# Kernel tuning notes

Hardware: AMD Instinct MI355X
Metric: run time of the kernel (lower is better)

The kernel has to match this reference:

```python
import jax, jax.numpy as jnp
import numpy as np

N_KNOTS = 16
DEGREE = 3
N_BASES = N_KNOTS - DEGREE - 1  # 12
F_CH = 128
KNOTS = jnp.linspace(0.0, 2.0, N_KNOTS, dtype=jnp.float32)


def bspline_basis(x, knots, degree):
    """Cox-de Boor B-spline basis. x: [...], returns [..., K-degree-1]."""
    K = knots.shape[0]
    xe = x[..., None]
    # degree-0 indicator basis: [..., K-1]
    b = ((xe >= knots[:-1]) & (xe < knots[1:])).astype(x.dtype)
    for d in range(1, degree + 1):
        left_den = knots[d:K - 1] - knots[:K - d - 1]
        right_den = knots[d + 1:K] - knots[1:K - d]
        safe_l = jnp.where(left_den > 0, left_den, 1.0)
        safe_r = jnp.where(right_den > 0, right_den, 1.0)
        left = jnp.where(left_den > 0, (xe - knots[:K - d - 1]) / safe_l, 0.0)
        right = jnp.where(right_den > 0, (knots[d + 1:K] - xe) / safe_r, 0.0)
        b = left * b[..., :K - d - 1] + right * b[..., 1:K - d]
    return b  # [..., K-degree-1]


def setup_inputs() -> dict:
    key = jax.random.key(0)
    k1, k2, k3 = jax.random.split(key, 3)
    B, N = 32, 8192
    eval_x = jax.random.normal(k1, (B, N, F_CH), dtype=jnp.float32)
    eval_eigs = jax.random.uniform(k2, (B, N), dtype=jnp.float32)  # in [0,1) within knot span [0,2]
    filter_scale = 1.0
    filter_coeffs = jax.random.normal(k3, (N_BASES, F_CH), dtype=jnp.float32) * filter_scale
    return {"eval_x": eval_x, "eval_eigs": eval_eigs, "filter_coeffs": filter_coeffs}


def reference(eval_x, eval_eigs, filter_coeffs):
    # basis: [B, N, n_bases]
    basis = bspline_basis(eval_eigs, KNOTS, DEGREE)
    # The torch split/cat/bmm/stack/transpose chain is exactly this contraction:
    # spectral_filter[b,n,f] = sum_k basis[b,n,k] * coeffs[k,f]
    spectral_filter = jnp.einsum('bnk,kf->bnf', basis, filter_coeffs)
    return eval_x * jnp.square(spectral_filter)
```

## Files before the change

kernel.cpp:

```cpp
#include <hip/hip_runtime.h>


#define N_BASES 12
#define F_CH 128
#define CHUNKS 2
#define ROW_VF4 (F_CH / 4)

typedef float vf4 __attribute__((ext_vector_type(4)));

template <bool EXACT>
__global__ __launch_bounds__(256, 8) void spline_filter_kernel(
    const vf4* __restrict__ x4,
    const float* __restrict__ eigs,
    const vf4* __restrict__ coeffs4,
    vf4*       __restrict__ out4,
    int total4, int stride4)
{
    const int gid = blockIdx.x * 256 + threadIdx.x;

    float eg[CHUNKS];
    vf4   xv[CHUNKS];

    #pragma unroll
    for (int c = 0; c < CHUNKS; ++c) {
        const int idx = gid + c * stride4;
        if (EXACT || idx < total4) eg[c] = eigs[idx >> 5];
        else                       eg[c] = 0.0f;
    }
    #pragma unroll
    for (int c = 0; c < CHUNKS; ++c) {
        const int idx = gid + c * stride4;
        if (EXACT || idx < total4) xv[c] = __builtin_nontemporal_load(&x4[idx]);
        else                       xv[c] = (vf4)0.0f;
    }

    const int lane = gid & 31;

    #pragma unroll
    for (int c = 0; c < CHUNKS; ++c) {
        const int idx = gid + c * stride4;
        if (!EXACT && idx >= total4) continue;

        float u = eg[c] * 7.5f;
        u = fminf(fmaxf(u, 0.0f), 15.0f);
        const int   i  = (int)u;
        const float tt = u - (float)i;
        const float t2  = tt * tt;
        const float t3  = t2 * tt;
        const float omt = 1.0f - tt;
        float w[4];
        w[0] = omt * omt * omt * (1.0f / 6.0f);
        w[1] = (3.0f * t3 - 6.0f * t2 + 4.0f) * (1.0f / 6.0f);
        w[2] = (-3.0f * t3 + 3.0f * t2 + 3.0f * tt + 1.0f) * (1.0f / 6.0f);
        w[3] = t3 * (1.0f / 6.0f);

        vf4 sf = (vf4)0.0f;
        #pragma unroll
        for (int j = 0; j < 4; ++j) {
            const int k  = i - 3 + j;
            const int kc = min(max(k, 0), N_BASES - 1);
            const float wj = (k == kc) ? w[j] : 0.0f;
            sf += wj * coeffs4[kc * ROW_VF4 + lane];
        }

        const vf4 o = xv[c] * sf * sf;
        __builtin_nontemporal_store(o, &out4[idx]);
    }
}

extern "C" void kernel_launch(void* const* d_in, const int* in_sizes, int n_in,
                              void* d_out, int out_size, void* d_ws, size_t ws_size,
                              hipStream_t stream) {
    const float* eval_x = (const float*)d_in[0];
    const float* eigs   = (const float*)d_in[1];
    const float* coeffs = (const float*)d_in[2];
    float* out = (float*)d_out;

    const int total4  = in_sizes[0] / 4;
    const int blocks  = (total4 + 256 * CHUNKS - 1) / (256 * CHUNKS);
    const int stride4 = blocks * 256;
    const bool exact  = (blocks * 256 * CHUNKS == total4);

    if (exact) {
        spline_filter_kernel<true><<<blocks, 256, 0, stream>>>(
            (const vf4*)eval_x, eigs, (const vf4*)coeffs, (vf4*)out,
            total4, stride4);
    } else {
        spline_filter_kernel<false><<<blocks, 256, 0, stream>>>(
            (const vf4*)eval_x, eigs, (const vf4*)coeffs, (vf4*)out,
            total4, stride4);
    }
}
```

Measured before the change: 226.1 us.

## Use fixed-size grid-stride loop with one-ahead prefetch of inputs

```diff
diff --git a/kernel.cpp b/kernel.cpp
--- a/kernel.cpp
+++ b/kernel.cpp
@@ -3,67 +3,82 @@
 
 #define N_BASES 12
 #define F_CH 128
-#define CHUNKS 2
+#define THREADS 256
+#define BLOCKS 2048
 #define ROW_VF4 (F_CH / 4)
 
 typedef float vf4 __attribute__((ext_vector_type(4)));
 
-template <bool EXACT>
-__global__ __launch_bounds__(256, 8) void spline_filter_kernel(
+__device__ __forceinline__ vf4 eval_sf(float eg, int lane,
+                                       const vf4* __restrict__ coeffs4) {
+    float u = eg * 7.5f;
+    u = fminf(fmaxf(u, 0.0f), 15.0f);
+    const int   i  = (int)u;
+    const float tt = u - (float)i;
+    const float t2  = tt * tt;
+    const float t3  = t2 * tt;
+    const float omt = 1.0f - tt;
+    float w[4];
+    w[0] = omt * omt * omt * (1.0f / 6.0f);
+    w[1] = (3.0f * t3 - 6.0f * t2 + 4.0f) * (1.0f / 6.0f);
+    w[2] = (-3.0f * t3 + 3.0f * t2 + 3.0f * tt + 1.0f) * (1.0f / 6.0f);
+    w[3] = t3 * (1.0f / 6.0f);
+
+    vf4 sf = (vf4)0.0f;
+    #pragma unroll
+    for (int j = 0; j < 4; ++j) {
+        const int k  = i - 3 + j;
+        const int kc = min(max(k, 0), N_BASES - 1);
+        const float wj = (k == kc) ? w[j] : 0.0f;
+        sf += wj * coeffs4[kc * ROW_VF4 + lane];
+    }
+    return sf;
+}
+
+template <int ITERS>
+__global__ __launch_bounds__(THREADS, 8) void spline_filter_exact(
+    const vf4* __restrict__ x4,
+    const float* __restrict__ eigs,
+    const vf4* __restrict__ coeffs4,
+    vf4*       __restrict__ out4)
+{
+    const int gid    = blockIdx.x * THREADS + threadIdx.x;
+    const int stride = BLOCKS * THREADS;
+    const int lane   = gid & 31;
+
+    int idx = gid;
+    float eg_n = eigs[idx >> 5];
+    vf4   xv_n = __builtin_nontemporal_load(&x4[idx]);
+
+    #pragma unroll
+    for (int it = 0; it < ITERS; ++it) {
+        const float eg = eg_n;
+        const vf4   xv = xv_n;
+        const int cur  = idx;
+        idx += stride;
+        if (it + 1 < ITERS) {
+            eg_n = eigs[idx >> 5];
+            xv_n = __builtin_nontemporal_load(&x4[idx]);
+        }
+        const vf4 sf = eval_sf(eg, lane, coeffs4);
+        const vf4 o  = xv * sf * sf;
+        __builtin_nontemporal_store(o, &out4[cur]);
+    }
+}
+
+__global__ __launch_bounds__(THREADS, 8) void spline_filter_generic(
     const vf4* __restrict__ x4,
     const float* __restrict__ eigs,
     const vf4* __restrict__ coeffs4,
     vf4*       __restrict__ out4,
-    int total4, int stride4)
+    int total4)
 {
-    const int gid = blockIdx.x * 256 + threadIdx.x;
-
-    float eg[CHUNKS];
-    vf4   xv[CHUNKS];
-
-    #pragma unroll
-    for (int c = 0; c < CHUNKS; ++c) {
-        const int idx = gid + c * stride4;
-        if (EXACT || idx < total4) eg[c] = eigs[idx >> 5];
-        else                       eg[c] = 0.0f;
-    }
-    #pragma unroll
-    for (int c = 0; c < CHUNKS; ++c) {
-        const int idx = gid + c * stride4;
-        if (EXACT || idx < total4) xv[c] = __builtin_nontemporal_load(&x4[idx]);
-        else                       xv[c] = (vf4)0.0f;
-    }
-
-    const int lane = gid & 31;
-
-    #pragma unroll
-    for (int c = 0; c < CHUNKS; ++c) {
-        const int idx = gid + c * stride4;
-        if (!EXACT && idx >= total4) continue;
-
-        float u = eg[c] * 7.5f;
-        u = fminf(fmaxf(u, 0.0f), 15.0f);
-        const int   i  = (int)u;
-        const float tt = u - (float)i;
-        const float t2  = tt * tt;
-        const float t3  = t2 * tt;
-        const float omt = 1.0f - tt;
-        float w[4];
-        w[0] = omt * omt * omt * (1.0f / 6.0f);
-        w[1] = (3.0f * t3 - 6.0f * t2 + 4.0f) * (1.0f / 6.0f);
-        w[2] = (-3.0f * t3 + 3.0f * t2 + 3.0f * tt + 1.0f) * (1.0f / 6.0f);
-        w[3] = t3 * (1.0f / 6.0f);
-
-        vf4 sf = (vf4)0.0f;
-        #pragma unroll
-        for (int j = 0; j < 4; ++j) {
-            const int k  = i - 3 + j;
-            const int kc = min(max(k, 0), N_BASES - 1);
-            const float wj = (k == kc) ? w[j] : 0.0f;
-            sf += wj * coeffs4[kc * ROW_VF4 + lane];
-        }
-
-        const vf4 o = xv[c] * sf * sf;
+    const int stride = gridDim.x * THREADS;
+    for (int idx = blockIdx.x * THREADS + threadIdx.x; idx < total4; idx += stride) {
+        const float eg = eigs[idx >> 5];
+        const vf4   xv = __builtin_nontemporal_load(&x4[idx]);
+        const vf4   sf = eval_sf(eg, idx & 31, coeffs4);
+        const vf4   o  = xv * sf * sf;
         __builtin_nontemporal_store(o, &out4[idx]);
     }
 }
@@ -76,18 +91,14 @@
     const float* coeffs = (const float*)d_in[2];
     float* out = (float*)d_out;
 
-    const int total4  = in_sizes[0] / 4;
-    const int blocks  = (total4 + 256 * CHUNKS - 1) / (256 * CHUNKS);
-    const int stride4 = blocks * 256;
-    const bool exact  = (blocks * 256 * CHUNKS == total4);
+    const int total4 = in_sizes[0] / 4;
 
-    if (exact) {
-        spline_filter_kernel<true><<<blocks, 256, 0, stream>>>(
-            (const vf4*)eval_x, eigs, (const vf4*)coeffs, (vf4*)out,
-            total4, stride4);
+    if (total4 == BLOCKS * THREADS * 16) {
+        spline_filter_exact<16><<<BLOCKS, THREADS, 0, stream>>>(
+            (const vf4*)eval_x, eigs, (const vf4*)coeffs, (vf4*)out);
     } else {
-        spline_filter_kernel<false><<<blocks, 256, 0, stream>>>(
-            (const vf4*)eval_x, eigs, (const vf4*)coeffs, (vf4*)out,
-            total4, stride4);
+        const int blocks = min((total4 + THREADS - 1) / THREADS, BLOCKS);
+        spline_filter_generic<<<blocks, THREADS, 0, stream>>>(
+            (const vf4*)eval_x, eigs, (const vf4*)coeffs, (vf4*)out, total4);
     }
 }
```

After: 229.7 us. Within noise of the previous version (+1.6%).
